# Performance work log

Hardware: AMD Instinct MI355X
Metric: run time of the kernel (lower is better)

The kernel has to match this reference:

```python
import jax, jax.numpy as jnp
import numpy as np

N_NODES = 100000
N_EDGES = 3200000
SIGMA_REF = 0.07
T_REF = 293.15
DSIGMA_DT = -0.0001
PHI_THRESH = 0.3
EPS = 1e-8


def compute_gradient(T, pos, edge_index):
    """Edge-based finite-difference gradient, scatter-reduced to nodes.

    grad_T[i] = mean over incoming edges (src->i) of
                (T[src]-T[i]) * (pos[src]-pos[i]) / |pos[src]-pos[i]|^2
    """
    src, dst = edge_index[0], edge_index[1]
    dT = T[src] - T[dst]                         # [E]
    dpos = pos[src] - pos[dst]                   # [E,3]
    dist2 = jnp.sum(dpos * dpos, axis=-1) + EPS  # [E]
    contrib = (dT / dist2)[:, None] * dpos       # [E,3]
    num = jax.ops.segment_sum(contrib, dst, num_segments=N_NODES)            # [N,3]
    cnt = jax.ops.segment_sum(jnp.ones_like(dT), dst, num_segments=N_NODES)  # [N]
    return num / jnp.maximum(cnt, 1.0)[:, None]


def setup_inputs() -> dict:
    key = jax.random.key(0)
    k1, k2, k3 = jax.random.split(key, 3)
    x = jax.random.normal(k1, (N_NODES, 9), dtype=jnp.float32)
    pos = jax.random.normal(k2, (N_NODES, 3), dtype=jnp.float32)
    edge_index = jax.random.randint(k3, (2, N_EDGES), 0, N_NODES, dtype=jnp.int64)
    return {"x": x, "pos": pos, "edge_index": edge_index}


def reference(x, pos, edge_index):
    T = x[:, 3]
    phi = x[:, 8]
    grad_T = compute_gradient(T, pos, edge_index)          # [N,3]
    force = DSIGMA_DT * grad_T                             # [N,3]
    interface_mask = (jnp.abs(phi) < PHI_THRESH).astype(force.dtype)
    return force * interface_mask[:, None]
```

## Files before the change

### kernel.cpp

```cpp
#include <hip/hip_runtime.h>

#define N_NODES 100000
#define N_EDGES 3200000
#define NVEC    (N_EDGES / 4)

#define S_LOG2  8
#define S       (1 << S_LOG2)
#define NPART   ((N_NODES + S - 1) / S)
#define NPB     448
#define GSTRIDE 16
#define NXCD    8
#define CAP8    1536

#define BT      1024
#define EPB     6252
#define NB      ((N_EDGES + EPB - 1) / EPB)
#define CAP     9216

constexpr float DSIGMA_DT  = -0.0001f;
constexpr float PHI_THRESH = 0.3f;
constexpr float EPS        = 1e-8f;

__global__ __launch_bounds__(BT, 8) void bin_kernel(const int4* __restrict__ ei4,
                                                    const float* __restrict__ x,
                                                    const float* __restrict__ pos,
                                                    float4* __restrict__ posT,
                                                    int* __restrict__ gcur,
                                                    int* __restrict__ buckets) {
    __shared__ int   lbuf[EPB];
    __shared__ unsigned short lrk[EPB];
    __shared__ unsigned short lbinS[EPB];
    __shared__ int hist[NPB], lofs[NPB];
    __shared__ int baseg[NPART];
    const int tid = threadIdx.x;
    const int xcd = blockIdx.x & (NXCD - 1);

    {
        const int per = (N_NODES + NB - 1) / NB;
        const int lo = blockIdx.x * per;
        const int hi = min(lo + per, N_NODES);
        for (int i = lo + tid; i < hi; i += BT)
            posT[i] = make_float4(pos[3 * i], pos[3 * i + 1], pos[3 * i + 2],
                                  x[9 * i + 3]);
    }

    const int ebase = blockIdx.x * EPB;
    const int n  = min(EPB, N_EDGES - ebase);
    const int nv = n >> 2;
    const int4* __restrict__ src4 = ei4 + (ebase >> 2);
    const int4* __restrict__ dst4 = ei4 + NVEC + (ebase >> 2);

    for (int i = tid; i < NPB; i += BT) hist[i] = 0;
    __syncthreads();

    for (int v = tid; v < nv; v += BT) {
        int4 d = dst4[v];
        ushort4 rk;
        rk.x = (unsigned short)atomicAdd(&hist[d.x >> S_LOG2], 1);
        rk.y = (unsigned short)atomicAdd(&hist[d.y >> S_LOG2], 1);
        rk.z = (unsigned short)atomicAdd(&hist[d.z >> S_LOG2], 1);
        rk.w = (unsigned short)atomicAdd(&hist[d.w >> S_LOG2], 1);
        ((ushort4*)lrk)[v] = rk;
    }
    __syncthreads();

    if (tid < 64) {
        int carry = 0;
        for (int b = 0; b < NPB; b += 64) {
            int v = hist[b + tid];
            int orig = v;
#pragma unroll
            for (int d = 1; d < 64; d <<= 1) {
                int t = __shfl_up(v, d, 64);
                if (tid >= d) v += t;
            }
            lofs[b + tid] = carry + v - orig;
            carry += __shfl(v, 63, 64);
        }
    }
    __syncthreads();
    if (tid < NPART)
        baseg[tid] = atomicAdd(&gcur[(xcd * NPART + tid) * GSTRIDE], hist[tid]);
    __syncthreads();

    for (int v = tid; v < nv; v += BT) {
        int4 s = src4[v];
        int4 d = dst4[v];
        ushort4 rk = ((const ushort4*)lrk)[v];
#pragma unroll
        for (int k = 0; k < 4; ++k) {
            int dk = k == 0 ? d.x : k == 1 ? d.y : k == 2 ? d.z : d.w;
            int sk = k == 0 ? s.x : k == 1 ? s.y : k == 2 ? s.z : s.w;
            int rr = k == 0 ? rk.x : k == 1 ? rk.y : k == 2 ? rk.z : rk.w;
            int bin = dk >> S_LOG2;
            int pos = lofs[bin] + rr;
            lbuf[pos]  = (sk << S_LOG2) | (dk & (S - 1));
            lbinS[pos] = (unsigned short)bin;
        }
    }
    __syncthreads();

    for (int i = tid; i < n; i += BT) {
        int b   = lbinS[i];
        int pos = baseg[b] + (i - lofs[b]);
        if (pos < CAP8)
            buckets[((size_t)(xcd * NPART + b)) * CAP8 + pos] = lbuf[i];
    }
}

__global__ __launch_bounds__(BT, 4) void part_kernel(
        const int* __restrict__ gcur,
        const int* __restrict__ buckets,
        const float4* __restrict__ posT,
        const float* __restrict__ x,
        float* __restrict__ out) {
    __shared__ int S2[CAP];
    __shared__ int hist[S], base[S];
    __shared__ float4 ploc[S];
    const int p = blockIdx.x, tid = threadIdx.x;
    const int lo = p << S_LOG2;

    if (tid < S) {
        hist[tid] = 0;
        int node = lo + tid;
        ploc[tid] = (node < N_NODES) ? posT[node] : make_float4(0.f, 0.f, 0.f, 0.f);
    }
    __syncthreads();

    int len[NXCD];
    int ent[NXCD][2];
    unsigned short prk[NXCD][2];
#pragma unroll
    for (int xx = 0; xx < NXCD; ++xx) {
        len[xx] = min(gcur[(xx * NPART + p) * GSTRIDE], CAP8);
        const int* __restrict__ bp = buckets + ((size_t)(xx * NPART + p)) * CAP8;
#pragma unroll
        for (int r = 0; r < 2; ++r) {
            int i = tid + r * BT;
            if (i < len[xx]) {
                int e = bp[i];
                ent[xx][r] = e;
                prk[xx][r] = (unsigned short)atomicAdd(&hist[e & (S - 1)], 1);
            }
        }
    }
    __syncthreads();

    if (tid < 64) {
        int carry = 0;
        for (int b = 0; b < S; b += 64) {
            int v = hist[b + tid];
            int orig = v;
#pragma unroll
            for (int d = 1; d < 64; d <<= 1) {
                int t = __shfl_up(v, d, 64);
                if (tid >= d) v += t;
            }
            base[b + tid] = carry + v - orig;
            carry += __shfl(v, 63, 64);
        }
    }
    __syncthreads();

#pragma unroll
    for (int xx = 0; xx < NXCD; ++xx) {
#pragma unroll
        for (int r = 0; r < 2; ++r) {
            int i = tid + r * BT;
            if (i < len[xx]) {
                int e = ent[xx][r];
                int pos = base[e & (S - 1)] + (int)prk[xx][r];
                if (pos < CAP) S2[pos] = e >> S_LOG2;
            }
        }
    }
    __syncthreads();

    const int rr = tid >> 2, q = tid & 3;
    const int node = lo + rr;
    const int nseg = hist[rr];
    const int b0 = base[rr];
    const int jend = min(b0 + nseg, CAP);
    float4 b = ploc[rr];
    float ax = 0.f, ay = 0.f, az = 0.f;
    for (int jj = b0 + q; jj < jend; jj += 4) {
        float4 a = posT[S2[jj]];
        float px = a.x - b.x, py = a.y - b.y, pz = a.z - b.z;
        float dT = a.w - b.w;
        float w  = dT / (px * px + py * py + pz * pz + EPS);
        ax += w * px; ay += w * py; az += w * pz;
    }
    ax += __shfl_down(ax, 2, 64); ax += __shfl_down(ax, 1, 64);
    ay += __shfl_down(ay, 2, 64); ay += __shfl_down(ay, 1, 64);
    az += __shfl_down(az, 2, 64); az += __shfl_down(az, 1, 64);
    if (q == 0 && node < N_NODES) {
        float phi = x[node * 9 + 8];
        float cn = nseg > 1 ? (float)nseg : 1.0f;
        float m = (fabsf(phi) < PHI_THRESH) ? (DSIGMA_DT / cn) : 0.0f;
        out[3 * node]     = m * ax;
        out[3 * node + 1] = m * ay;
        out[3 * node + 2] = m * az;
    }
}

__global__ void prep_kernel(const float* __restrict__ x,
                            const float* __restrict__ pos,
                            float4* __restrict__ posT) {
    int i = blockIdx.x * blockDim.x + threadIdx.x;
    if (i < N_NODES)
        posT[i] = make_float4(pos[3 * i], pos[3 * i + 1], pos[3 * i + 2],
                              x[9 * i + 3]);
}

__global__ void edge_scatter_atomic_kernel(const int* __restrict__ ei,
                                           const float4* __restrict__ posT,
                                           float4* __restrict__ accum) {
    int e = blockIdx.x * blockDim.x + threadIdx.x;
    if (e >= N_EDGES) return;
    int s = ei[e];
    int d = ei[N_EDGES + e];
    float4 a = posT[s];
    float4 b = posT[d];
    float px = a.x - b.x, py = a.y - b.y, pz = a.z - b.z;
    float dT = a.w - b.w;
    float w  = dT / (px * px + py * py + pz * pz + EPS);
    float* ac = (float*)&accum[d];
    atomicAdd(ac,     w * px);
    atomicAdd(ac + 1, w * py);
    atomicAdd(ac + 2, w * pz);
    atomicAdd(ac + 3, 1.0f);
}

__global__ void finalize_accum_kernel(const float* __restrict__ x,
                                      const float4* __restrict__ accum,
                                      float* __restrict__ out) {
    int i = blockIdx.x * blockDim.x + threadIdx.x;
    if (i >= N_NODES) return;
    float4 a = accum[i];
    float phi = x[i * 9 + 8];
    float cn = a.w > 1.0f ? a.w : 1.0f;
    float m = (fabsf(phi) < PHI_THRESH) ? (DSIGMA_DT / cn) : 0.0f;
    out[3 * i]     = m * a.x;
    out[3 * i + 1] = m * a.y;
    out[3 * i + 2] = m * a.z;
}

extern "C" void kernel_launch(void* const* d_in, const int* in_sizes, int n_in,
                              void* d_out, int out_size, void* d_ws, size_t ws_size,
                              hipStream_t stream) {
    const float* x   = (const float*)d_in[0];
    const float* pos = (const float*)d_in[1];
    const int*   ei  = (const int*)d_in[2];
    float* out = (float*)d_out;

    const size_t posT_b = (size_t)N_NODES * sizeof(float4);
    const size_t gcur_b = (size_t)NXCD * NPART * GSTRIDE * sizeof(int);
    const size_t buck_b = (size_t)NXCD * NPART * CAP8 * sizeof(int);

    char* w = (char*)d_ws;
    float4* posT    = (float4*)w;
    int*    gcur    = (int*)(w + posT_b);
    int*    buckets = (int*)(w + posT_b + ((gcur_b + 255) & ~255ull));

    const size_t need_full = posT_b + ((gcur_b + 255) & ~255ull) + buck_b;

    const int B = 256;

    if (ws_size >= need_full) {
        hipMemsetAsync(gcur, 0, gcur_b, stream);
        bin_kernel<<<NB, BT, 0, stream>>>((const int4*)ei, x, pos, posT, gcur, buckets);
        part_kernel<<<NPART, BT, 0, stream>>>(gcur, buckets, posT, x, out);
    } else {
        float4* accum = (float4*)(w + posT_b);
        prep_kernel<<<(N_NODES + B - 1) / B, B, 0, stream>>>(x, pos, posT);
        hipMemsetAsync(accum, 0, (size_t)N_NODES * sizeof(float4), stream);
        edge_scatter_atomic_kernel<<<(N_EDGES + B - 1) / B, B, 0, stream>>>(ei, posT, accum);
        finalize_accum_kernel<<<(N_NODES + B - 1) / B, B, 0, stream>>>(x, accum, out);
    }
}
```

Baseline: 113.3 us.

## Keep edge chunks and ranks in registers in bin kernel, drop LDS rank array

The bin kernel now uses 512 threads and exactly 6144 edges per block, so each thread holds three int4 src/dst vectors and their 12 local ranks in registers. This removes the LDS rank array, the second global read of src/dst, and one __syncthreads between computing bin bases and scattering into LDS. The cost is higher register pressure. The fixed three-iteration unroll relies on EPB being exactly 3*512*4, and the block count changes slightly.

After: 114.4 us. No clear change (+1.0%).

```diff
diff --git a/kernel.cpp b/kernel.cpp
--- a/kernel.cpp
+++ b/kernel.cpp
@@ -12,23 +12,23 @@
 #define NXCD    8
 #define CAP8    1536
 
+#define EPB     6144
+#define NB      ((N_EDGES + EPB - 1) / EPB)
 #define BT      1024
-#define EPB     6252
-#define NB      ((N_EDGES + EPB - 1) / EPB)
 #define CAP     9216
 
 constexpr float DSIGMA_DT  = -0.0001f;
 constexpr float PHI_THRESH = 0.3f;
 constexpr float EPS        = 1e-8f;
 
-__global__ __launch_bounds__(BT, 8) void bin_kernel(const int4* __restrict__ ei4,
-                                                    const float* __restrict__ x,
-                                                    const float* __restrict__ pos,
-                                                    float4* __restrict__ posT,
-                                                    int* __restrict__ gcur,
-                                                    int* __restrict__ buckets) {
+__global__ __launch_bounds__(512, 6) void bin_kernel(
+        const int4* __restrict__ ei4,
+        const float* __restrict__ x,
+        const float* __restrict__ pos,
+        float4* __restrict__ posT,
+        int* __restrict__ gcur,
+        int* __restrict__ buckets) {
     __shared__ int   lbuf[EPB];
-    __shared__ unsigned short lrk[EPB];
     __shared__ unsigned short lbinS[EPB];
     __shared__ int hist[NPB], lofs[NPB];
     __shared__ int baseg[NPART];
@@ -39,7 +39,7 @@
         const int per = (N_NODES + NB - 1) / NB;
         const int lo = blockIdx.x * per;
         const int hi = min(lo + per, N_NODES);
-        for (int i = lo + tid; i < hi; i += BT)
+        for (int i = lo + tid; i < hi; i += 512)
             posT[i] = make_float4(pos[3 * i], pos[3 * i + 1], pos[3 * i + 2],
                                   x[9 * i + 3]);
     }
@@ -50,17 +50,22 @@
     const int4* __restrict__ src4 = ei4 + (ebase >> 2);
     const int4* __restrict__ dst4 = ei4 + NVEC + (ebase >> 2);
 
-    for (int i = tid; i < NPB; i += BT) hist[i] = 0;
-    __syncthreads();
-
-    for (int v = tid; v < nv; v += BT) {
-        int4 d = dst4[v];
-        ushort4 rk;
-        rk.x = (unsigned short)atomicAdd(&hist[d.x >> S_LOG2], 1);
-        rk.y = (unsigned short)atomicAdd(&hist[d.y >> S_LOG2], 1);
-        rk.z = (unsigned short)atomicAdd(&hist[d.z >> S_LOG2], 1);
-        rk.w = (unsigned short)atomicAdd(&hist[d.w >> S_LOG2], 1);
-        ((ushort4*)lrk)[v] = rk;
+    for (int i = tid; i < NPB; i += 512) hist[i] = 0;
+    __syncthreads();
+
+    int4 rs[3], rd[3];
+    unsigned short rk[12];
+#pragma unroll
+    for (int k = 0; k < 3; ++k) {
+        int v = tid + k * 512;
+        if (v < nv) {
+            rs[k] = src4[v];
+            rd[k] = dst4[v];
+            rk[4 * k + 0] = (unsigned short)atomicAdd(&hist[rd[k].x >> S_LOG2], 1);
+            rk[4 * k + 1] = (unsigned short)atomicAdd(&hist[rd[k].y >> S_LOG2], 1);
+            rk[4 * k + 2] = (unsigned short)atomicAdd(&hist[rd[k].z >> S_LOG2], 1);
+            rk[4 * k + 3] = (unsigned short)atomicAdd(&hist[rd[k].w >> S_LOG2], 1);
+        }
     }
     __syncthreads();
 
@@ -81,26 +86,25 @@
     __syncthreads();
     if (tid < NPART)
         baseg[tid] = atomicAdd(&gcur[(xcd * NPART + tid) * GSTRIDE], hist[tid]);
-    __syncthreads();
-
-    for (int v = tid; v < nv; v += BT) {
-        int4 s = src4[v];
-        int4 d = dst4[v];
-        ushort4 rk = ((const ushort4*)lrk)[v];
-#pragma unroll
-        for (int k = 0; k < 4; ++k) {
-            int dk = k == 0 ? d.x : k == 1 ? d.y : k == 2 ? d.z : d.w;
-            int sk = k == 0 ? s.x : k == 1 ? s.y : k == 2 ? s.z : s.w;
-            int rr = k == 0 ? rk.x : k == 1 ? rk.y : k == 2 ? rk.z : rk.w;
-            int bin = dk >> S_LOG2;
-            int pos = lofs[bin] + rr;
-            lbuf[pos]  = (sk << S_LOG2) | (dk & (S - 1));
-            lbinS[pos] = (unsigned short)bin;
-        }
-    }
-    __syncthreads();
-
-    for (int i = tid; i < n; i += BT) {
+
+#pragma unroll
+    for (int k = 0; k < 3; ++k) {
+        int v = tid + k * 512;
+        if (v < nv) {
+#pragma unroll
+            for (int j = 0; j < 4; ++j) {
+                int dk = j == 0 ? rd[k].x : j == 1 ? rd[k].y : j == 2 ? rd[k].z : rd[k].w;
+                int sk = j == 0 ? rs[k].x : j == 1 ? rs[k].y : j == 2 ? rs[k].z : rs[k].w;
+                int bin = dk >> S_LOG2;
+                int pos = lofs[bin] + (int)rk[4 * k + j];
+                lbuf[pos]  = (sk << S_LOG2) | (dk & (S - 1));
+                lbinS[pos] = (unsigned short)bin;
+            }
+        }
+    }
+    __syncthreads();
+
+    for (int i = tid; i < n; i += 512) {
         int b   = lbinS[i];
         int pos = baseg[b] + (i - lofs[b]);
         if (pos < CAP8)
@@ -268,7 +272,7 @@
 
     if (ws_size >= need_full) {
         hipMemsetAsync(gcur, 0, gcur_b, stream);
-        bin_kernel<<<NB, BT, 0, stream>>>((const int4*)ei, x, pos, posT, gcur, buckets);
+        bin_kernel<<<NB, 512, 0, stream>>>((const int4*)ei, x, pos, posT, gcur, buckets);
         part_kernel<<<NPART, BT, 0, stream>>>(gcur, buckets, posT, x, out);
     } else {
         float4* accum = (float4*)(w + posT_b);
```
